# Optimization experiments

Hardware: AMD Instinct MI355X
Metric: run time of the kernel (lower is better)

The kernel has to match this reference:

```python
import jax, jax.numpy as jnp
import numpy as np

EMB, HEADS, LEVELS, POINTS = 256, 8, 4, 4
DHEAD = EMB // HEADS
SHAPES = [(128, 128), (64, 64), (32, 32), (16, 16)]  # (H, W) per level
S = sum(h * w for h, w in SHAPES)  # 21760 flattened multiscale tokens
B, Q = 2, S
LN_EPS = 1e-5


def setup_inputs() -> dict:
    key = jax.random.key(0)
    ks = jax.random.split(key, 10)
    f = lambda k, shp, s=0.02: jax.random.normal(k, shp, jnp.float32) * s
    return {
        "img_feat": jax.random.normal(ks[0], (B, S, EMB), jnp.float32),
        "img_shapes": jnp.array(SHAPES, jnp.int32),
        "img_mask": jnp.zeros((B, S), bool),  # True = padded
        "img_valid_ratios": jnp.ones((B, LEVELS, 2), jnp.float32),
        "query_feat": jax.random.normal(ks[1], (B, Q, EMB), jnp.float32),
        "query_pos": jax.random.normal(ks[2], (B, Q, EMB), jnp.float32),
        "query_points": jax.random.uniform(ks[3], (B, Q, 2), jnp.float32),
        "W_value": f(ks[4], (EMB, EMB)), "b_value": jnp.zeros((EMB,), jnp.float32),
        "W_off": f(ks[5], (EMB, HEADS * LEVELS * POINTS * 2)),
        "b_off": f(ks[6], (HEADS * LEVELS * POINTS * 2,), 0.5),
        "W_attn": f(ks[7], (EMB, HEADS * LEVELS * POINTS)),
        "b_attn": jnp.zeros((HEADS * LEVELS * POINTS,), jnp.float32),
        "W_out": f(ks[8], (EMB, EMB)), "b_out": jnp.zeros((EMB,), jnp.float32),
        "ln_gamma": jnp.ones((EMB,), jnp.float32), "ln_beta": jnp.zeros((EMB,), jnp.float32),
    }


def reference(img_feat, img_shapes, img_mask, img_valid_ratios, query_feat, query_pos,
              query_points, W_value, b_value, W_off, b_off, W_attn, b_attn, W_out, b_out,
              ln_gamma, ln_beta):
    Bq, Qn = query_feat.shape[:2]
    # value projection + padding mask, split heads: [B, S, H, D]
    v = img_feat @ W_value + b_value
    v = jnp.where(img_mask[:, :, None], 0.0, v).reshape(Bq, -1, HEADS, DHEAD)
    q = query_feat + query_pos  # position-modulated query
    off = (q @ W_off + b_off).reshape(Bq, Qn, HEADS, LEVELS, POINTS, 2)
    attn = jax.nn.softmax((q @ W_attn + b_attn).reshape(Bq, Qn, HEADS, LEVELS * POINTS), -1)
    attn = attn.reshape(Bq, Qn, HEADS, LEVELS, POINTS)
    # reference points scaled by per-level valid ratios: [B, Q, L, 2] (x, y in [0,1])
    ref = query_points[:, :, None, :] * img_valid_ratios[:, None, :, :]
    bb = jnp.arange(Bq)[:, None, None, None]
    hh = jnp.arange(HEADS)[None, None, :, None]
    out = jnp.zeros((Bq, Qn, HEADS, DHEAD), q.dtype)
    start = 0
    for l, (H, W) in enumerate(SHAPES):
        norm = jnp.array([W, H], q.dtype)
        loc = ref[:, :, None, l, None, :] + off[:, :, :, l] / norm  # [B,Q,H,P,2]
        # grid_sample align_corners=False pixel coords
        x = loc[..., 0] * W - 0.5
        y = loc[..., 1] * H - 0.5
        x0 = jnp.floor(x); y0 = jnp.floor(y)
        wx = x - x0; wy = y - y0
        x0i = x0.astype(jnp.int32); y0i = y0.astype(jnp.int32)
        samp = jnp.zeros((Bq, Qn, HEADS, POINTS, DHEAD), q.dtype)
        for dx, dy, w in ((0, 0, (1 - wx) * (1 - wy)), (1, 0, wx * (1 - wy)),
                          (0, 1, (1 - wx) * wy), (1, 1, wx * wy)):
            xi = x0i + dx; yi = y0i + dy
            ok = (xi >= 0) & (xi < W) & (yi >= 0) & (yi < H)  # zero padding
            idx = start + jnp.clip(yi, 0, H - 1) * W + jnp.clip(xi, 0, W - 1)
            samp = samp + (w * ok)[..., None] * v[bb, idx, hh, :]
        out = out + jnp.einsum('bqhp,bqhpd->bqhd', attn[:, :, :, l], samp)
        start += H * W
    update = out.reshape(Bq, Qn, EMB) @ W_out + b_out
    # SkipConnection: LayerNorm(skip + dropout(update)), dropout p=0
    x = query_feat + update
    mu = x.mean(-1, keepdims=True)
    var = ((x - mu) ** 2).mean(-1, keepdims=True)
    return (x - mu) * jax.lax.rsqrt(var + LN_EPS) * ln_gamma + ln_beta
```

## Files before the change

### kernel.cpp

```cpp
#include <hip/hip_runtime.h>
#include <hip/hip_bf16.h>

#define EMB 256
#define SEQ 21760
#define NB 2
#define NROW (NB * SEQ)
#define QB 8
#define LN_EPS 1e-5f

typedef __hip_bfloat16 bf16;
typedef short bf16x8 __attribute__((ext_vector_type(8)));
typedef float f32x4 __attribute__((ext_vector_type(4)));

__device__ __forceinline__ unsigned short f2bf(float f) {
  __hip_bfloat16 h = __float2bfloat16(f);
  return *reinterpret_cast<unsigned short*>(&h);
}
__device__ __forceinline__ float bf2f(unsigned short u) {
  return __uint_as_float((unsigned int)u << 16);
}
__device__ __forceinline__ float bflo(unsigned int u) { return __uint_as_float(u << 16); }
__device__ __forceinline__ float bfhi(unsigned int u) { return __uint_as_float(u & 0xffff0000u); }

__global__ __launch_bounds__(256) void k_trans(const float* __restrict__ src,
                                               unsigned short* __restrict__ dst, int N) {
  const int n = blockIdx.x, k = threadIdx.x;
  dst[n * 256 + k] = f2bf(src[k * N + n]);
}

__global__ __launch_bounds__(256) void k_value(const float* __restrict__ A,
                                               const unsigned short* __restrict__ Wt,
                                               const float* __restrict__ bias,
                                               const unsigned char* __restrict__ mask,
                                               bf16* __restrict__ V) {
  __shared__ unsigned short As[64 * 256];
  const int tid = threadIdx.x;
  const int lane = tid & 63, w = tid >> 6;
  const int row0 = blockIdx.x * 64;
#pragma unroll
  for (int it = 0; it < 8; ++it) {
    const int cid = it * 256 + tid;
    const int row = cid >> 5, c = cid & 31;
    const float4* p = (const float4*)(A + (size_t)(row0 + row) * 256 + c * 8);
    const float4 a0 = p[0], a1 = p[1];
    union { unsigned short u[8]; uint4 q; } pk;
    pk.u[0] = f2bf(a0.x); pk.u[1] = f2bf(a0.y); pk.u[2] = f2bf(a0.z); pk.u[3] = f2bf(a0.w);
    pk.u[4] = f2bf(a1.x); pk.u[5] = f2bf(a1.y); pk.u[6] = f2bf(a1.z); pk.u[7] = f2bf(a1.w);
    *(uint4*)((char*)As + row * 512 + ((c * 16) ^ ((row & 7) << 4))) = pk.q;
  }
  __syncthreads();
  const int lg16 = lane >> 4, l16 = lane & 15;
  f32x4 acc[4][4] = {};
#pragma unroll
  for (int kk = 0; kk < 8; ++kk) {
    bf16x8 af[4], bh[4];
#pragma unroll
    for (int mf = 0; mf < 4; ++mf) {
      const int row = mf * 16 + l16;
      af[mf] = *(const bf16x8*)((const char*)As + row * 512 +
                                ((kk * 64 + lg16 * 16) ^ ((row & 7) << 4)));
    }
#pragma unroll
    for (int nf = 0; nf < 4; ++nf) {
      const int col = w * 64 + nf * 16 + l16;
      bh[nf] = *(const bf16x8*)(Wt + (size_t)col * 256 + kk * 32 + lg16 * 8);
    }
#pragma unroll
    for (int mf = 0; mf < 4; ++mf)
#pragma unroll
      for (int nf = 0; nf < 4; ++nf)
        acc[mf][nf] = __builtin_amdgcn_mfma_f32_16x16x32_bf16(af[mf], bh[nf], acc[mf][nf], 0, 0, 0);
  }
#pragma unroll
  for (int mf = 0; mf < 4; ++mf) {
    const int rbase = mf * 16 + lg16 * 4;
    const uchar4 mk = *(const uchar4*)(mask + row0 + rbase);
#pragma unroll
    for (int nf = 0; nf < 4; ++nf) {
      const int col = w * 64 + nf * 16 + l16;
      const int hh = col >> 5, ch = col & 31;
      const float bb = bias[col];
#pragma unroll
      for (int r = 0; r < 4; ++r) {
        const unsigned char m = (r == 0) ? mk.x : (r == 1) ? mk.y : (r == 2) ? mk.z : mk.w;
        const float v = m ? 0.f : (acc[mf][nf][r] + bb);
        V[(size_t)hh * (NROW * 32) + (size_t)(row0 + rbase + r) * 32 + ch] =
            __float2bfloat16(v);
      }
    }
  }
}

__global__ __launch_bounds__(256) void k_offattn(const float* __restrict__ qf,
                                                 const float* __restrict__ qp,
                                                 const unsigned short* __restrict__ Wt,
                                                 const float* __restrict__ boff,
                                                 const float* __restrict__ battn,
                                                 bf16* __restrict__ off,
                                                 bf16* __restrict__ lg) {
  __shared__ unsigned short As[64 * 256];
  const int tid = threadIdx.x;
  const int lane = tid & 63, w = tid >> 6;
  const int row0 = blockIdx.x * 64;
#pragma unroll
  for (int it = 0; it < 8; ++it) {
    const int cid = it * 256 + tid;
    const int row = cid >> 5, c = cid & 31;
    const float4* pf = (const float4*)(qf + (size_t)(row0 + row) * 256 + c * 8);
    const float4* pp = (const float4*)(qp + (size_t)(row0 + row) * 256 + c * 8);
    const float4 a0 = pf[0], a1 = pf[1], b0 = pp[0], b1 = pp[1];
    union { unsigned short u[8]; uint4 q; } pk;
    pk.u[0] = f2bf(a0.x + b0.x); pk.u[1] = f2bf(a0.y + b0.y);
    pk.u[2] = f2bf(a0.z + b0.z); pk.u[3] = f2bf(a0.w + b0.w);
    pk.u[4] = f2bf(a1.x + b1.x); pk.u[5] = f2bf(a1.y + b1.y);
    pk.u[6] = f2bf(a1.z + b1.z); pk.u[7] = f2bf(a1.w + b1.w);
    *(uint4*)((char*)As + row * 512 + ((c * 16) ^ ((row & 7) << 4))) = pk.q;
  }
  __syncthreads();
  const int lg16 = lane >> 4, l16 = lane & 15;
  f32x4 acc[4][6] = {};
#pragma unroll
  for (int kk = 0; kk < 8; ++kk) {
    bf16x8 af[4], bh[6];
#pragma unroll
    for (int mf = 0; mf < 4; ++mf) {
      const int row = mf * 16 + l16;
      af[mf] = *(const bf16x8*)((const char*)As + row * 512 +
                                ((kk * 64 + lg16 * 16) ^ ((row & 7) << 4)));
    }
#pragma unroll
    for (int nf = 0; nf < 6; ++nf) {
      const int col = w * 96 + nf * 16 + l16;
      bh[nf] = *(const bf16x8*)(Wt + (size_t)col * 256 + kk * 32 + lg16 * 8);
    }
#pragma unroll
    for (int mf = 0; mf < 4; ++mf)
#pragma unroll
      for (int nf = 0; nf < 6; ++nf)
        acc[mf][nf] = __builtin_amdgcn_mfma_f32_16x16x32_bf16(af[mf], bh[nf], acc[mf][nf], 0, 0, 0);
  }
#pragma unroll
  for (int mf = 0; mf < 4; ++mf) {
    const int rbase = row0 + mf * 16 + lg16 * 4;
#pragma unroll
    for (int nf = 0; nf < 6; ++nf) {
      const int col = w * 96 + nf * 16 + l16;
      if (col < 256) {
        const float bb = boff[col];
#pragma unroll
        for (int r = 0; r < 4; ++r)
          off[(size_t)(rbase + r) * 256 + col] = __float2bfloat16(acc[mf][nf][r] + bb);
      } else {
        const float bb = battn[col - 256];
#pragma unroll
        for (int r = 0; r < 4; ++r)
          lg[(size_t)(rbase + r) * 128 + (col - 256)] = __float2bfloat16(acc[mf][nf][r] + bb);
      }
    }
  }
}

__global__ __launch_bounds__(256) void k_sample(const bf16* __restrict__ V,
                                                const bf16* off,
                                                const bf16* __restrict__ lg,
                                                const float* __restrict__ qpts,
                                                const float* __restrict__ vratio,
                                                unsigned short* samp) {
  __shared__ uint2 sIdx[QB * 16 * 9];
  __shared__ uint2 sW[QB * 16 * 9];
  __shared__ float sMax[QB * 8], sInv[QB * 8];
  const int t = threadIdx.x;
  const int row0 = blockIdx.x * QB;

  if (t < QB * 8) {
    const int q = t >> 3, h = t & 7;
    const int row = row0 + q;
    const uint4* lp = (const uint4*)(lg + (size_t)row * 128 + h * 16);
    uint4 u0 = lp[0], u1 = lp[1];
    float v[16];
    v[0] = bflo(u0.x); v[1] = bfhi(u0.x); v[2] = bflo(u0.y); v[3] = bfhi(u0.y);
    v[4] = bflo(u0.z); v[5] = bfhi(u0.z); v[6] = bflo(u0.w); v[7] = bfhi(u0.w);
    v[8] = bflo(u1.x); v[9] = bfhi(u1.x); v[10] = bflo(u1.y); v[11] = bfhi(u1.y);
    v[12] = bflo(u1.z); v[13] = bfhi(u1.z); v[14] = bflo(u1.w); v[15] = bfhi(u1.w);
    float m = v[0];
#pragma unroll
    for (int i = 1; i < 16; ++i) m = fmaxf(m, v[i]);
    float s = 0.f;
#pragma unroll
    for (int i = 0; i < 16; ++i) s += __expf(v[i] - m);
    sMax[t] = m;
    sInv[t] = 1.f / s;
  }
  __syncthreads();

  const int Wl_[4] = {128, 64, 32, 16};
  const int st_[4] = {0, 16384, 20480, 21504};
#pragma unroll
  for (int tt = 0; tt < 4; ++tt) {
    const int sid = t + tt * 256;
    const int q = sid >> 7, s = sid & 127;
    const int h = s >> 4, i = s & 15, l = i >> 2;
    const int row = row0 + q;
    const int b = row >= SEQ;
    const unsigned int u = *(const unsigned int*)(off + (size_t)row * 256 + s * 2);
    const float ox = bflo(u), oy = bfhi(u);
    const float lgv = bf2f(*(const unsigned short*)(lg + (size_t)row * 128 + s));
    const float e = __expf(lgv - sMax[q * 8 + h]) * sInv[q * 8 + h];
    const float px = qpts[(size_t)row * 2], py = qpts[(size_t)row * 2 + 1];
    const float vrx = vratio[b * 8 + l * 2], vry = vratio[b * 8 + l * 2 + 1];
    const int Wl = Wl_[l];
    const float fW = (float)Wl;
    const float x = fmaf(px * vrx, fW, ox) - 0.5f;
    const float y = fmaf(py * vry, fW, oy) - 0.5f;
    const float fx = floorf(x), fy = floorf(y);
    const float wx = x - fx, wy = y - fy;
    const int x0 = (int)fx, y0 = (int)fy;
    const int x1 = x0 + 1, y1 = y0 + 1;
    const int xc0 = min(max(x0, 0), Wl - 1), xc1 = min(max(x1, 0), Wl - 1);
    const int yc0 = min(max(y0, 0), Wl - 1), yc1 = min(max(y1, 0), Wl - 1);
    const float ox0 = (x0 >= 0 && x0 < Wl) ? e : 0.f;
    const float ox1 = (x1 >= 0 && x1 < Wl) ? e : 0.f;
    const float oy0 = (y0 >= 0 && y0 < Wl) ? 1.f : 0.f;
    const float oy1 = (y1 >= 0 && y1 < Wl) ? 1.f : 0.f;
    const int base = b * SEQ + st_[l];
    const int r0 = base + yc0 * Wl, r1 = base + yc1 * Wl;
    uint2 I, Wp;
    I.x = (unsigned int)(r0 + xc0) | ((unsigned int)(r0 + xc1) << 16);
    I.y = (unsigned int)(r1 + xc0) | ((unsigned int)(r1 + xc1) << 16);
    Wp.x = (unsigned int)f2bf((1.f - wx) * (1.f - wy) * ox0 * oy0) |
           ((unsigned int)f2bf(wx * (1.f - wy) * ox1 * oy0) << 16);
    Wp.y = (unsigned int)f2bf((1.f - wx) * wy * ox0 * oy1) |
           ((unsigned int)f2bf(wx * wy * ox1 * oy1) << 16);
    sIdx[(q * 16 + i) * 9 + h] = I;
    sW[(q * 16 + i) * 9 + h] = Wp;
  }
  __syncthreads();

  const int q = t >> 5, sub = t & 31;
  const int h = sub >> 2, dg = sub & 3;
  const int row = row0 + q;
  const bf16* vb = V + (size_t)h * (NROW * 32) + dg * 8;
  float a0 = 0.f, a1 = 0.f, a2 = 0.f, a3 = 0.f;
  float a4 = 0.f, a5 = 0.f, a6 = 0.f, a7 = 0.f;
#pragma unroll
  for (int i = 0; i < 16; ++i) {
    const uint2 I = sIdx[(q * 16 + i) * 9 + h];
    const uint2 Wp = sW[(q * 16 + i) * 9 + h];
    const int i0 = I.x & 0xffff, i1 = I.x >> 16;
    const int i2 = I.y & 0xffff, i3 = I.y >> 16;
    const float w0 = bflo(Wp.x), w1 = bfhi(Wp.x);
    const float w2 = bflo(Wp.y), w3 = bfhi(Wp.y);
    {
      const uint4 u = *(const uint4*)(vb + (size_t)i0 * 32);
      a0 = fmaf(w0, bflo(u.x), a0); a1 = fmaf(w0, bfhi(u.x), a1);
      a2 = fmaf(w0, bflo(u.y), a2); a3 = fmaf(w0, bfhi(u.y), a3);
      a4 = fmaf(w0, bflo(u.z), a4); a5 = fmaf(w0, bfhi(u.z), a5);
      a6 = fmaf(w0, bflo(u.w), a6); a7 = fmaf(w0, bfhi(u.w), a7);
    }
    {
      const uint4 u = *(const uint4*)(vb + (size_t)i1 * 32);
      a0 = fmaf(w1, bflo(u.x), a0); a1 = fmaf(w1, bfhi(u.x), a1);
      a2 = fmaf(w1, bflo(u.y), a2); a3 = fmaf(w1, bfhi(u.y), a3);
      a4 = fmaf(w1, bflo(u.z), a4); a5 = fmaf(w1, bfhi(u.z), a5);
      a6 = fmaf(w1, bflo(u.w), a6); a7 = fmaf(w1, bfhi(u.w), a7);
    }
    {
      const uint4 u = *(const uint4*)(vb + (size_t)i2 * 32);
      a0 = fmaf(w2, bflo(u.x), a0); a1 = fmaf(w2, bfhi(u.x), a1);
      a2 = fmaf(w2, bflo(u.y), a2); a3 = fmaf(w2, bfhi(u.y), a3);
      a4 = fmaf(w2, bflo(u.z), a4); a5 = fmaf(w2, bfhi(u.z), a5);
      a6 = fmaf(w2, bflo(u.w), a6); a7 = fmaf(w2, bfhi(u.w), a7);
    }
    {
      const uint4 u = *(const uint4*)(vb + (size_t)i3 * 32);
      a0 = fmaf(w3, bflo(u.x), a0); a1 = fmaf(w3, bfhi(u.x), a1);
      a2 = fmaf(w3, bflo(u.y), a2); a3 = fmaf(w3, bfhi(u.y), a3);
      a4 = fmaf(w3, bflo(u.z), a4); a5 = fmaf(w3, bfhi(u.z), a5);
      a6 = fmaf(w3, bflo(u.w), a6); a7 = fmaf(w3, bfhi(u.w), a7);
    }
  }
  uint4 pk;
  pk.x = (unsigned int)f2bf(a0) | ((unsigned int)f2bf(a1) << 16);
  pk.y = (unsigned int)f2bf(a2) | ((unsigned int)f2bf(a3) << 16);
  pk.z = (unsigned int)f2bf(a4) | ((unsigned int)f2bf(a5) << 16);
  pk.w = (unsigned int)f2bf(a6) | ((unsigned int)f2bf(a7) << 16);
  *(uint4*)((char*)samp + (size_t)row * 512 + (h * 32 + dg * 8) * 2) = pk;
}

__global__ __launch_bounds__(256) void k_upd(const unsigned short* __restrict__ A,
                                             const unsigned short* __restrict__ Wt,
                                             const float* __restrict__ bias,
                                             bf16* __restrict__ U) {
  __shared__ unsigned short As[64 * 256];
  const int tid = threadIdx.x;
  const int lane = tid & 63, w = tid >> 6;
  const int row0 = blockIdx.x * 64;
#pragma unroll
  for (int it = 0; it < 8; ++it) {
    const int cid = it * 256 + tid;
    const int row = cid >> 5, c = cid & 31;
    const uint4 q = *(const uint4*)(A + (size_t)(row0 + row) * 256 + c * 8);
    *(uint4*)((char*)As + row * 512 + ((c * 16) ^ ((row & 7) << 4))) = q;
  }
  __syncthreads();
  const int lg16 = lane >> 4, l16 = lane & 15;
  f32x4 acc[4][4] = {};
#pragma unroll
  for (int kk = 0; kk < 8; ++kk) {
    bf16x8 af[4], bh[4];
#pragma unroll
    for (int mf = 0; mf < 4; ++mf) {
      const int row = mf * 16 + l16;
      af[mf] = *(const bf16x8*)((const char*)As + row * 512 +
                                ((kk * 64 + lg16 * 16) ^ ((row & 7) << 4)));
    }
#pragma unroll
    for (int nf = 0; nf < 4; ++nf) {
      const int col = w * 64 + nf * 16 + l16;
      bh[nf] = *(const bf16x8*)(Wt + (size_t)col * 256 + kk * 32 + lg16 * 8);
    }
#pragma unroll
    for (int mf = 0; mf < 4; ++mf)
#pragma unroll
      for (int nf = 0; nf < 4; ++nf)
        acc[mf][nf] = __builtin_amdgcn_mfma_f32_16x16x32_bf16(af[mf], bh[nf], acc[mf][nf], 0, 0, 0);
  }
#pragma unroll
  for (int mf = 0; mf < 4; ++mf) {
    const int rbase = row0 + mf * 16 + lg16 * 4;
#pragma unroll
    for (int nf = 0; nf < 4; ++nf) {
      const int col = w * 64 + nf * 16 + l16;
      const float bb = bias[col];
#pragma unroll
      for (int r = 0; r < 4; ++r)
        U[(size_t)(rbase + r) * 256 + col] = __float2bfloat16(acc[mf][nf][r] + bb);
    }
  }
}

__global__ __launch_bounds__(256) void k_ln(const unsigned short* __restrict__ upd,
                                            const float* __restrict__ qf,
                                            const float* __restrict__ gamma,
                                            const float* __restrict__ beta,
                                            float* __restrict__ y) {
  const int w = threadIdx.x >> 6, lane = threadIdx.x & 63;
  const int row = blockIdx.x * 4 + w;
  const int c = lane * 4;
  const ushort4 u = *(const ushort4*)(upd + (size_t)row * 256 + c);
  const float4 qv = *(const float4*)(qf + (size_t)row * 256 + c);
  const float x0 = qv.x + bf2f(u.x);
  const float x1 = qv.y + bf2f(u.y);
  const float x2 = qv.z + bf2f(u.z);
  const float x3 = qv.w + bf2f(u.w);
  float s1 = x0 + x1 + x2 + x3;
  float s2 = x0 * x0 + x1 * x1 + x2 * x2 + x3 * x3;
#pragma unroll
  for (int o = 32; o >= 1; o >>= 1) {
    s1 += __shfl_xor(s1, o);
    s2 += __shfl_xor(s2, o);
  }
  const float mu = s1 * (1.f / 256.f);
  const float var = s2 * (1.f / 256.f) - mu * mu;
  const float rsig = rsqrtf(var + LN_EPS);
  const float4 g = *(const float4*)(gamma + c);
  const float4 bt = *(const float4*)(beta + c);
  float4 o;
  o.x = (x0 - mu) * rsig * g.x + bt.x;
  o.y = (x1 - mu) * rsig * g.y + bt.y;
  o.z = (x2 - mu) * rsig * g.z + bt.z;
  o.w = (x3 - mu) * rsig * g.w + bt.w;
  *(float4*)(y + (size_t)row * 256 + c) = o;
}

extern "C" void kernel_launch(void* const* d_in, const int* in_sizes, int n_in,
                              void* d_out, int out_size, void* d_ws, size_t ws_size,
                              hipStream_t stream) {
  const float* img_feat = (const float*)d_in[0];
  const unsigned char* img_mask = (const unsigned char*)d_in[2];
  const float* vratio = (const float*)d_in[3];
  const float* qf = (const float*)d_in[4];
  const float* qp = (const float*)d_in[5];
  const float* qpts = (const float*)d_in[6];
  const float* Wv = (const float*)d_in[7];
  const float* bv = (const float*)d_in[8];
  const float* Woff = (const float*)d_in[9];
  const float* boff = (const float*)d_in[10];
  const float* Wattn = (const float*)d_in[11];
  const float* battn = (const float*)d_in[12];
  const float* Wout = (const float*)d_in[13];
  const float* bout = (const float*)d_in[14];
  const float* gamma = (const float*)d_in[15];
  const float* beta = (const float*)d_in[16];

  char* ws = (char*)d_ws;
  bf16* V = (bf16*)ws;
  bf16* off = (bf16*)(ws + (size_t)NROW * 256 * 2);
  bf16* lg = (bf16*)(ws + (size_t)NROW * 256 * 4);
  unsigned short* wbase =
      (unsigned short*)(ws + (size_t)NROW * 256 * 4 + (size_t)NROW * 128 * 2);
  unsigned short* WvT = wbase;
  unsigned short* WcatT = WvT + 65536;
  unsigned short* WoutT = WcatT + 98304;

  dim3 blk(256);
  k_trans<<<256, blk, 0, stream>>>(Wv, WvT, 256);
  k_trans<<<256, blk, 0, stream>>>(Woff, WcatT, 256);
  k_trans<<<128, blk, 0, stream>>>(Wattn, WcatT + 256 * 256, 128);
  k_trans<<<256, blk, 0, stream>>>(Wout, WoutT, 256);
  k_value<<<NROW / 64, blk, 0, stream>>>(img_feat, WvT, bv, img_mask, V);
  k_offattn<<<NROW / 64, blk, 0, stream>>>(qf, qp, WcatT, boff, battn, off, lg);
  k_sample<<<NROW / QB, blk, 0, stream>>>(V, off, lg, qpts, vratio,
                                          (unsigned short*)off );
  k_upd<<<NROW / 64, blk, 0, stream>>>((const unsigned short*)off , WoutT,
                                       bout, V );
  k_ln<<<NROW / 4, blk, 0, stream>>>((const unsigned short*)V, qf, gamma, beta,
                                     (float*)d_out);
}
```

Baseline: 214.1 us.

## Split k_sample blocks per head with 64 queries each

The sampling kernel's work is repartitioned so each block handles one head for 64 consecutive queries, instead of all 8 heads for 8 queries. Shared index and weight tables become per-query rows padded to 17 entries, and the grid grows to 8 × (NROW/64) blocks. The aim is better cache locality: neighbouring queries gather from nearby locations within a single head's contiguous value plane. Pointers are also marked __restrict__ even though off and samp alias the same buffer. Each block still reads only its own head's columns before writing them, but the restrict qualifier is technically unsafe.

Measured after the change: 195.0 us. -8.9%, faster.

```diff
diff --git a/kernel.cpp b/kernel.cpp
--- a/kernel.cpp
+++ b/kernel.cpp
@@ -5,7 +5,6 @@
 #define SEQ 21760
 #define NB 2
 #define NROW (NB * SEQ)
-#define QB 8
 #define LN_EPS 1e-5f
 
 typedef __hip_bfloat16 bf16;
@@ -161,20 +160,20 @@
 }
 
 __global__ __launch_bounds__(256) void k_sample(const bf16* __restrict__ V,
-                                                const bf16* off,
+                                                const bf16* __restrict__ off,
                                                 const bf16* __restrict__ lg,
                                                 const float* __restrict__ qpts,
                                                 const float* __restrict__ vratio,
-                                                unsigned short* samp) {
-  __shared__ uint2 sIdx[QB * 16 * 9];
-  __shared__ uint2 sW[QB * 16 * 9];
-  __shared__ float sMax[QB * 8], sInv[QB * 8];
+                                                unsigned short* __restrict__ samp) {
+  __shared__ uint2 sIdx[64 * 17];
+  __shared__ uint2 sW[64 * 17];
+  __shared__ float sMax[64], sInv[64];
   const int t = threadIdx.x;
-  const int row0 = blockIdx.x * QB;
-
-  if (t < QB * 8) {
-    const int q = t >> 3, h = t & 7;
-    const int row = row0 + q;
+  const int h = blockIdx.x & 7;
+  const int row0 = (blockIdx.x >> 3) * 64;
+
+  if (t < 64) {
+    const int row = row0 + t;
     const uint4* lp = (const uint4*)(lg + (size_t)row * 128 + h * 16);
     uint4 u0 = lp[0], u1 = lp[1];
     float v[16];
@@ -198,14 +197,13 @@
 #pragma unroll
   for (int tt = 0; tt < 4; ++tt) {
     const int sid = t + tt * 256;
-    const int q = sid >> 7, s = sid & 127;
-    const int h = s >> 4, i = s & 15, l = i >> 2;
+    const int q = sid >> 4, i = sid & 15, l = i >> 2;
     const int row = row0 + q;
     const int b = row >= SEQ;
-    const unsigned int u = *(const unsigned int*)(off + (size_t)row * 256 + s * 2);
+    const unsigned int u = *(const unsigned int*)(off + (size_t)row * 256 + (h * 16 + i) * 2);
     const float ox = bflo(u), oy = bfhi(u);
-    const float lgv = bf2f(*(const unsigned short*)(lg + (size_t)row * 128 + s));
-    const float e = __expf(lgv - sMax[q * 8 + h]) * sInv[q * 8 + h];
+    const float lgv = bf2f(*(const unsigned short*)(lg + (size_t)row * 128 + h * 16 + i));
+    const float e = __expf(lgv - sMax[q]) * sInv[q];
     const float px = qpts[(size_t)row * 2], py = qpts[(size_t)row * 2 + 1];
     const float vrx = vratio[b * 8 + l * 2], vry = vratio[b * 8 + l * 2 + 1];
     const int Wl = Wl_[l];
@@ -231,21 +229,20 @@
            ((unsigned int)f2bf(wx * (1.f - wy) * ox1 * oy0) << 16);
     Wp.y = (unsigned int)f2bf((1.f - wx) * wy * ox0 * oy1) |
            ((unsigned int)f2bf(wx * wy * ox1 * oy1) << 16);
-    sIdx[(q * 16 + i) * 9 + h] = I;
-    sW[(q * 16 + i) * 9 + h] = Wp;
+    sIdx[q * 17 + i] = I;
+    sW[q * 17 + i] = Wp;
   }
   __syncthreads();
 
-  const int q = t >> 5, sub = t & 31;
-  const int h = sub >> 2, dg = sub & 3;
+  const int q = t >> 2, dg = t & 3;
   const int row = row0 + q;
   const bf16* vb = V + (size_t)h * (NROW * 32) + dg * 8;
   float a0 = 0.f, a1 = 0.f, a2 = 0.f, a3 = 0.f;
   float a4 = 0.f, a5 = 0.f, a6 = 0.f, a7 = 0.f;
 #pragma unroll
   for (int i = 0; i < 16; ++i) {
-    const uint2 I = sIdx[(q * 16 + i) * 9 + h];
-    const uint2 Wp = sW[(q * 16 + i) * 9 + h];
+    const uint2 I = sIdx[q * 17 + i];
+    const uint2 Wp = sW[q * 17 + i];
     const int i0 = I.x & 0xffff, i1 = I.x >> 16;
     const int i2 = I.y & 0xffff, i3 = I.y >> 16;
     const float w0 = bflo(Wp.x), w1 = bfhi(Wp.x);
@@ -410,8 +407,8 @@
   k_trans<<<256, blk, 0, stream>>>(Wout, WoutT, 256);
   k_value<<<NROW / 64, blk, 0, stream>>>(img_feat, WvT, bv, img_mask, V);
   k_offattn<<<NROW / 64, blk, 0, stream>>>(qf, qp, WcatT, boff, battn, off, lg);
-  k_sample<<<NROW / QB, blk, 0, stream>>>(V, off, lg, qpts, vratio,
-                                          (unsigned short*)off );
+  k_sample<<<8 * (NROW / 64), blk, 0, stream>>>(V, off, lg, qpts, vratio,
+                                                (unsigned short*)off );
   k_upd<<<NROW / 64, blk, 0, stream>>>((const unsigned short*)off , WoutT,
                                        bout, V );
   k_ln<<<NROW / 4, blk, 0, stream>>>((const unsigned short*)V, qf, gamma, beta,
```
